# Performance work log

Measured on AMD Instinct MI355X. Metric: run time of the kernel, lower is better.

Reference implementation:

```python
import jax, jax.numpy as jnp
import numpy as np

HIDDEN = 2048
FFN = 1024
NUM_EXPERTS = 64
TOP_K = 8
TOTAL_EXPERTS = NUM_EXPERTS + TOP_K  # trash-can experts appended


def setup_inputs() -> dict:
    key = jax.random.key(0)
    ks = jax.random.split(key, 5)
    hidden_states = jax.random.normal(ks[0], (4, 2048, HIDDEN), dtype=jnp.float32)
    # gate: [total_experts, hidden]
    gate_w = jax.random.normal(ks[1], (TOTAL_EXPERTS, HIDDEN), dtype=jnp.float32) * 0.02
    # OlmoeMLP (SwiGLU): gate_proj, up_proj: [E, hidden, ffn]; down_proj: [E, ffn, hidden]
    w_gate = jax.random.normal(ks[2], (NUM_EXPERTS, HIDDEN, FFN), dtype=jnp.float32) * 0.02
    w_up = jax.random.normal(ks[3], (NUM_EXPERTS, HIDDEN, FFN), dtype=jnp.float32) * 0.02
    w_down = jax.random.normal(ks[4], (NUM_EXPERTS, FFN, HIDDEN), dtype=jnp.float32) * 0.02
    return {"hidden_states": hidden_states, "gate_w": gate_w,
            "w_gate": w_gate, "w_up": w_up, "w_down": w_down}


def _moe_forward(hidden_states, gate_w, w_gate, w_up, w_down):
    b, s, h = hidden_states.shape
    x = hidden_states.reshape(-1, h)  # [T, H]
    router_logits = x @ gate_w.T  # [T, total_experts]
    routing_weights = jax.nn.softmax(router_logits.astype(jnp.float32), axis=-1)
    topk_w, topk_idx = jax.lax.top_k(routing_weights, TOP_K)  # [T, K]
    # norm_topk_prob = False -> no renorm
    topk_w = topk_w.astype(hidden_states.dtype)

    # Dense-equivalent combine honoring sparsity via per-expert mask-weighted sum:
    # combine_w[t, e] = sum of topk weights where topk_idx==e, zero for trash experts.
    onehot = jax.nn.one_hot(topk_idx, TOTAL_EXPERTS, dtype=topk_w.dtype)  # [T,K,E_tot]
    combine_w = jnp.einsum('tk,tke->te', topk_w, onehot)[:, :NUM_EXPERTS]  # [T,E]

    # Grouped expert compute (vectorized over experts).
    # For correctness baseline we compute each expert on all tokens and weight;
    # zero weights kill non-routed tokens (same math as gather/scatter).
    def one_expert(wg, wu, wd, w_col):
        inter = jax.nn.silu(x @ wg) * (x @ wu)  # [T, FFN]
        return (inter @ wd) * w_col[:, None]    # [T, H]

    out = jnp.zeros_like(x)
    # scan over experts to cap peak memory at one [T,FFN] intermediate
    def body(acc, args):
        wg, wu, wd, w_col = args
        return acc + one_expert(wg, wu, wd, w_col), None
    out, _ = jax.lax.scan(body, out, (w_gate, w_up, w_down, combine_w.T))
    return out.reshape(b, s, h), router_logits


def reference(hidden_states, gate_w, w_gate, w_up, w_down):
    return _moe_forward(hidden_states, gate_w, w_gate, w_up, w_down)
```

## Files before the change

### kernel.cpp

```cpp
#include <hip/hip_runtime.h>
#include <hip/hip_bf16.h>
#include <stdint.h>

#define T_TOK 8192
#define HID   2048
#define FFN   1024
#define NEXP  64
#define ETOT  72
#define NPAD  80
#define TOPK  8
#define NASSIGN (T_TOK*TOPK)
#define ECHUNK 16

typedef unsigned short u16;
typedef __bf16 bf16;
typedef bf16 bf16x8 __attribute__((ext_vector_type(8)));
typedef float f32x4 __attribute__((ext_vector_type(4)));

typedef const __attribute__((address_space(1))) void* gp_t;
typedef __attribute__((address_space(3))) void* lp_t;

__device__ __forceinline__ void gload16(const void* g, void* lds) {
  __builtin_amdgcn_global_load_lds((gp_t)g, (lp_t)lds, 16, 0, 0);
}

__device__ __forceinline__ f32x4 mfma16(bf16x8 a, bf16x8 b, f32x4 c) {
  return __builtin_amdgcn_mfma_f32_16x16x32_bf16(a, b, c, 0, 0, 0);
}

union U8 { bf16 h[8]; uint4 u; };
union U2 { bf16 h[2]; unsigned int u; };

__global__ void k_prep_x(const float* __restrict__ x, u16* __restrict__ xh,
                         u16* __restrict__ xl, int n8) {
  int i = blockIdx.x * blockDim.x + threadIdx.x;
  int stride = gridDim.x * blockDim.x;
  for (; i < n8; i += stride) {
    const float4* p = (const float4*)(x + (size_t)i * 8);
    float4 a = p[0], b = p[1];
    float f[8] = {a.x,a.y,a.z,a.w,b.x,b.y,b.z,b.w};
    U8 hh, ll;
#pragma unroll
    for (int j = 0; j < 8; j++) {
      bf16 h = (bf16)f[j];
      hh.h[j] = h;
      ll.h[j] = (bf16)(f[j] - (float)h);
    }
    ((uint4*)xh)[i] = hh.u;
    ((uint4*)xl)[i] = ll.u;
  }
}

__global__ void k_prep_gate(const float* __restrict__ gw, u16* __restrict__ gh,
                            u16* __restrict__ gl) {
  int e = blockIdx.x;
  for (int k8 = threadIdx.x; k8 < HID/8; k8 += blockDim.x) {
    U8 hh, ll;
    if (e < ETOT) {
      const float4* p = (const float4*)(gw + (size_t)e*HID + k8*8);
      float4 a = p[0], b = p[1];
      float f[8] = {a.x,a.y,a.z,a.w,b.x,b.y,b.z,b.w};
#pragma unroll
      for (int j = 0; j < 8; j++) {
        bf16 h = (bf16)f[j]; hh.h[j] = h; ll.h[j] = (bf16)(f[j]-(float)h);
      }
    } else {
      hh.u = make_uint4(0,0,0,0); ll.u = make_uint4(0,0,0,0);
    }
    ((uint4*)gh)[(size_t)e*(HID/8) + k8] = hh.u;
    ((uint4*)gl)[(size_t)e*(HID/8) + k8] = ll.u;
  }
}

__global__ void k_convT(const float* __restrict__ src, u16* __restrict__ dst,
                        int R, int C) {
  int e = blockIdx.z;
  src += (size_t)e * R * C;
  dst += (size_t)e * R * C;
  int c0 = blockIdx.x * 64, r0 = blockIdx.y * 128;
  __shared__ u16 t[64 * 132];
  int tid = threadIdx.x;
  int rr = tid >> 4, cc = (tid & 15) * 4;
#pragma unroll
  for (int it = 0; it < 8; it++) {
    int r = it * 16 + rr;
    float4 v = *(const float4*)(src + (size_t)(r0 + r) * C + c0 + cc);
    const float* f = &v.x;
#pragma unroll
    for (int i = 0; i < 4; i++) {
      U2 u; u.h[0] = (bf16)f[i]; u.h[1] = (bf16)0.f;
      t[(cc + i) * 132 + r] = (u16)(u.u & 0xffffu);
    }
  }
  __syncthreads();
  int n = tid >> 2, kb = (tid & 3) * 32;
  u16* drow = dst + (size_t)(c0 + n) * R + r0 + kb;
  const u16* srow = &t[n * 132 + kb];
#pragma unroll
  for (int j = 0; j < 2; j++) {
    uint2 a = *(const uint2*)&srow[j*16 + 0];
    uint2 b = *(const uint2*)&srow[j*16 + 4];
    uint2 c = *(const uint2*)&srow[j*16 + 8];
    uint2 d = *(const uint2*)&srow[j*16 + 12];
    *(uint4*)&drow[j*16]     = make_uint4(a.x, a.y, b.x, b.y);
    *(uint4*)&drow[j*16 + 8] = make_uint4(c.x, c.y, d.x, d.y);
  }
}

__global__ void k_router(const u16* __restrict__ xh, const u16* __restrict__ xl,
                         const u16* __restrict__ gh, const u16* __restrict__ gl,
                         float* __restrict__ logits_out, int* __restrict__ tk_idx,
                         float* __restrict__ tk_w, int* __restrict__ counts) {
  __shared__ u16 la_h[64*32], la_l[64*32], lb_h[NPAD*32], lb_l[NPAD*32];
  __shared__ float llog[64*NPAD];
  int tid = threadIdx.x, lane = tid & 63, wid = tid >> 6;
  int t0 = blockIdx.x * 64;
  int rsub = lane >> 2, csub = lane & 3;
  f32x4 acc[5] = {};
#pragma unroll 1
  for (int k0 = 0; k0 < HID; k0 += 32) {
    int arow = wid*16 + rsub;
    gload16(xh + (size_t)(t0+arow)*HID + k0 + csub*8, &la_h[wid*512]);
    gload16(xl + (size_t)(t0+arow)*HID + k0 + csub*8, &la_l[wid*512]);
    int brow = wid*16 + rsub;
    gload16(gh + (size_t)brow*HID + k0 + csub*8, &lb_h[wid*512]);
    gload16(gl + (size_t)brow*HID + k0 + csub*8, &lb_l[wid*512]);
    if (wid == 0) gload16(gh + (size_t)(64+rsub)*HID + k0 + csub*8, &lb_h[4*512]);
    if (wid == 1) gload16(gl + (size_t)(64+rsub)*HID + k0 + csub*8, &lb_l[4*512]);
    __syncthreads();
    int ar = wid*16 + (lane & 15);
    int ks = lane >> 4;
    bf16x8 ah = *(const bf16x8*)&la_h[ar*32 + ks*8];
    bf16x8 al = *(const bf16x8*)&la_l[ar*32 + ks*8];
#pragma unroll
    for (int nf = 0; nf < 5; nf++) {
      int br = nf*16 + (lane & 15);
      bf16x8 bh = *(const bf16x8*)&lb_h[br*32 + ks*8];
      bf16x8 bl = *(const bf16x8*)&lb_l[br*32 + ks*8];
      acc[nf] = mfma16(ah, bh, acc[nf]);
      acc[nf] = mfma16(ah, bl, acc[nf]);
      acc[nf] = mfma16(al, bh, acc[nf]);
    }
    __syncthreads();
  }
  {
    int q = lane >> 4, c = lane & 15;
#pragma unroll
    for (int nf = 0; nf < 5; nf++)
#pragma unroll
      for (int r = 0; r < 4; r++)
        llog[(wid*16 + q*4 + r)*NPAD + nf*16 + c] = acc[nf][r];
  }
  __syncthreads();
  if (tid < 64) {
    int t = t0 + tid;
    float* lg = &llog[tid*NPAD];
    float m = -1e30f;
    for (int e = 0; e < ETOT; e++) {
      float v = lg[e];
      logits_out[(size_t)t*ETOT + e] = v;
      m = fmaxf(m, v);
    }
    float s = 0.f;
    for (int e = 0; e < ETOT; e++) s += __expf(lg[e] - m);
    uint64_t m0 = 0; unsigned int m1 = 0;
    for (int k = 0; k < TOPK; k++) {
      float best = -1e30f; int bi = 0;
      for (int e = 0; e < ETOT; e++) {
        bool used = (e < 64) ? ((m0 >> e) & 1) : ((m1 >> (e-64)) & 1);
        float v = lg[e];
        if (!used && v > best) { best = v; bi = e; }
      }
      if (bi < 64) m0 |= (1ull << bi); else m1 |= (1u << (bi-64));
      tk_idx[t*TOPK + k] = bi;
      tk_w[t*TOPK + k] = __expf(best - m) / s;
      if (bi < NEXP) atomicAdd(&counts[bi], 1);
    }
  }
}

__global__ void k_scan(const int* __restrict__ counts, int* __restrict__ offsets,
                       int* __restrict__ cursors) {
  if (threadIdx.x == 0) {
    int s = 0;
    for (int e = 0; e < NEXP; e++) { offsets[e] = s; cursors[e] = s; s += counts[e]; }
  }
}

__global__ void k_build(const int* __restrict__ tk_idx, const float* __restrict__ tk_w,
                        int* __restrict__ cursors, int* __restrict__ rows,
                        float* __restrict__ rwgt) {
  int t = blockIdx.x * blockDim.x + threadIdx.x;
  if (t >= T_TOK) return;
#pragma unroll
  for (int k = 0; k < TOPK; k++) {
    int e = tk_idx[t*TOPK + k];
    if (e < NEXP) {
      int p = atomicAdd(&cursors[e], 1);
      rows[p] = t;
      rwgt[p] = tk_w[t*TOPK + k];
    }
  }
}

__launch_bounds__(256, 2)
__global__ void k_expert_gu(const u16* __restrict__ xh, const u16* __restrict__ wgT,
                            const u16* __restrict__ wuT, const int* __restrict__ counts,
                            const int* __restrict__ offsets, const int* __restrict__ rows,
                            u16* __restrict__ inter, int e0) {
  int ez = blockIdx.z, e = e0 + ez, nb = blockIdx.y;
  int cnt = counts[e];
  if (cnt == 0) return;
  int off = offsets[e];
  int n0 = nb * 128;
  int tid = threadIdx.x, lane = tid & 63, wid = tid >> 6;
  int wm = (wid >> 1) * 64, wn = (wid & 1) * 64;
  __shared__ u16 la[128*32], lbg[128*32], lbu[128*32];
  __shared__ u16 lout[128*128];
  int rsub = lane >> 2, csub = lane & 3;
  int swzc = csub ^ ((rsub >> 1) & 3);
  int nr1 = wid*16 + rsub, nr2 = nr1 + 64;
  const u16* gb_g1 = wgT + ((size_t)ez*FFN + n0 + nr1)*HID + swzc*8;
  const u16* gb_g2 = wgT + ((size_t)ez*FFN + n0 + nr2)*HID + swzc*8;
  const u16* gb_u1 = wuT + ((size_t)ez*FFN + n0 + nr1)*HID + swzc*8;
  const u16* gb_u2 = wuT + ((size_t)ez*FFN + n0 + nr2)*HID + swzc*8;

  for (int m0 = blockIdx.x * 128; m0 < cnt; m0 += gridDim.x * 128) {
    int tok1 = (m0 + nr1 < cnt) ? rows[off + m0 + nr1] : 0;
    int tok2 = (m0 + nr2 < cnt) ? rows[off + m0 + nr2] : 0;
    const u16* ga1 = xh + (size_t)tok1*HID + swzc*8;
    const u16* ga2 = xh + (size_t)tok2*HID + swzc*8;
    f32x4 accg[4][4] = {}, accu[4][4] = {};
#pragma unroll 1
    for (int k0 = 0; k0 < HID; k0 += 32) {
      gload16(ga1 + k0, &la[wid*512]);
      gload16(ga2 + k0, &la[(wid+4)*512]);
      gload16(gb_g1 + k0, &lbg[wid*512]);
      gload16(gb_g2 + k0, &lbg[(wid+4)*512]);
      gload16(gb_u1 + k0, &lbu[wid*512]);
      gload16(gb_u2 + k0, &lbu[(wid+4)*512]);
      __syncthreads();
      bf16x8 afr[4], bgf[4], buf_[4];
#pragma unroll
      for (int i = 0; i < 4; i++) {
        int row = wm + i*16 + (lane & 15);
        int ch = (lane >> 4) ^ ((row >> 1) & 3);
        afr[i] = *(const bf16x8*)&la[row*32 + ch*8];
        int n = wn + i*16 + (lane & 15);
        int chb = (lane >> 4) ^ ((n >> 1) & 3);
        bgf[i]  = *(const bf16x8*)&lbg[n*32 + chb*8];
        buf_[i] = *(const bf16x8*)&lbu[n*32 + chb*8];
      }
#pragma unroll
      for (int nf = 0; nf < 4; nf++)
#pragma unroll
        for (int mf = 0; mf < 4; mf++) {
          accg[mf][nf] = mfma16(afr[mf], bgf[nf], accg[mf][nf]);
          accu[mf][nf] = mfma16(afr[mf], buf_[nf], accu[mf][nf]);
        }
      __syncthreads();
    }
#pragma unroll
    for (int mf = 0; mf < 4; mf++)
#pragma unroll
      for (int nf = 0; nf < 4; nf++)
#pragma unroll
        for (int r = 0; r < 4; r++) {
          float g = accg[mf][nf][r], u = accu[mf][nf][r];
          float v = g / (1.f + __expf(-g)) * u;
          int row = wm + mf*16 + (lane >> 4)*4 + r;
          int col = wn + nf*16 + (lane & 15);
          U2 t; t.h[0] = (bf16)v; t.h[1] = (bf16)0.f;
          lout[row*128 + col] = (u16)(t.u & 0xffffu);
        }
    __syncthreads();
    for (int idx = tid; idx < 2048; idx += 256) {
      int row = idx >> 4, c16 = idx & 15;
      if (m0 + row < cnt) {
        uint4 v = *(const uint4*)&lout[row*128 + c16*8];
        *(uint4*)&inter[(size_t)(off + m0 + row)*FFN + n0 + c16*8] = v;
      }
    }
    __syncthreads();
  }
}

__launch_bounds__(256, 2)
__global__ void k_expert_down(const u16* __restrict__ inter, const u16* __restrict__ wdT,
                              const int* __restrict__ counts, const int* __restrict__ offsets,
                              const int* __restrict__ rows, const float* __restrict__ rwgt,
                              float* __restrict__ out, int e0) {
  int ez = blockIdx.z, e = e0 + ez, nb = blockIdx.y;
  int cnt = counts[e];
  if (cnt == 0) return;
  int off = offsets[e];
  int n0 = nb * 128;
  int tid = threadIdx.x, lane = tid & 63, wid = tid >> 6;
  int wm = (wid >> 1) * 64, wn = (wid & 1) * 64;
  __shared__ u16 la[128*32], lb[128*32];
  __shared__ int rows_l[128];
  __shared__ float rw_l[128];
  int rsub = lane >> 2, csub = lane & 3;
  int swzc = csub ^ ((rsub >> 1) & 3);
  int nr1 = wid*16 + rsub, nr2 = nr1 + 64;
  const u16* gb1 = wdT + ((size_t)ez*HID + n0 + nr1)*FFN + swzc*8;
  const u16* gb2 = wdT + ((size_t)ez*HID + n0 + nr2)*FFN + swzc*8;

  for (int m0 = blockIdx.x * 128; m0 < cnt; m0 += gridDim.x * 128) {
    __syncthreads();
    if (tid < 128) {
      int r = m0 + tid;
      rows_l[tid] = (r < cnt) ? rows[off + r] : 0;
      rw_l[tid]   = (r < cnt) ? rwgt[off + r] : 0.f;
    }
    const u16* ga1 = inter + (size_t)(off + m0 + nr1)*FFN + swzc*8;
    const u16* ga2 = inter + (size_t)(off + m0 + nr2)*FFN + swzc*8;
    f32x4 acc[4][4] = {};
#pragma unroll 1
    for (int k0 = 0; k0 < FFN; k0 += 32) {
      gload16(ga1 + k0, &la[wid*512]);
      gload16(ga2 + k0, &la[(wid+4)*512]);
      gload16(gb1 + k0, &lb[wid*512]);
      gload16(gb2 + k0, &lb[(wid+4)*512]);
      __syncthreads();
      bf16x8 afr[4], bfr[4];
#pragma unroll
      for (int i = 0; i < 4; i++) {
        int row = wm + i*16 + (lane & 15);
        int ch = (lane >> 4) ^ ((row >> 1) & 3);
        afr[i] = *(const bf16x8*)&la[row*32 + ch*8];
        int n = wn + i*16 + (lane & 15);
        int chb = (lane >> 4) ^ ((n >> 1) & 3);
        bfr[i] = *(const bf16x8*)&lb[n*32 + chb*8];
      }
#pragma unroll
      for (int nf = 0; nf < 4; nf++)
#pragma unroll
        for (int mf = 0; mf < 4; mf++)
          acc[mf][nf] = mfma16(afr[mf], bfr[nf], acc[mf][nf]);
      __syncthreads();
    }
#pragma unroll
    for (int mf = 0; mf < 4; mf++)
#pragma unroll
      for (int nf = 0; nf < 4; nf++)
#pragma unroll
        for (int r = 0; r < 4; r++) {
          int row = wm + mf*16 + (lane >> 4)*4 + r;
          if (m0 + row < cnt) {
            int tok = rows_l[row];
            float w = rw_l[row];
            int col = n0 + wn + nf*16 + (lane & 15);
            atomicAdd(&out[(size_t)tok*HID + col], w * acc[mf][nf][r]);
          }
        }
  }
}

extern "C" void kernel_launch(void* const* d_in, const int* in_sizes, int n_in,
                              void* d_out, int out_size, void* d_ws, size_t ws_size,
                              hipStream_t stream) {
  const float* x      = (const float*)d_in[0];
  const float* gate_w = (const float*)d_in[1];
  const float* wg     = (const float*)d_in[2];
  const float* wu     = (const float*)d_in[3];
  const float* wd     = (const float*)d_in[4];
  float* out = (float*)d_out;
  float* logits_out = out + (size_t)T_TOK * HID;

  char* w = (char*)d_ws;
  u16* xh = (u16*)w;            w += (size_t)T_TOK*HID*2;
  u16* xl = (u16*)w;            w += (size_t)T_TOK*HID*2;
  u16* gh = (u16*)w;            w += (size_t)NPAD*HID*2;
  u16* gl = (u16*)w;            w += (size_t)NPAD*HID*2;
  int* tk_idx = (int*)w;        w += (size_t)T_TOK*TOPK*4;
  float* tk_w = (float*)w;      w += (size_t)T_TOK*TOPK*4;
  int* counts = (int*)w;        w += 256;
  int* offsets = (int*)w;       w += 256;
  int* cursors = (int*)w;       w += 256;
  int* rows = (int*)w;          w += (size_t)NASSIGN*4;
  float* rwgt = (float*)w;      w += (size_t)NASSIGN*4;
  u16* inter = (u16*)w;         w += ((size_t)NASSIGN + 128)*FFN*2;
  u16* wgT = (u16*)w;           w += (size_t)ECHUNK*FFN*HID*2;
  u16* wuT = (u16*)w;           w += (size_t)ECHUNK*FFN*HID*2;
  u16* wdT = (u16*)w;

  hipMemsetAsync(d_out, 0, (size_t)T_TOK*HID*4, stream);
  hipMemsetAsync(counts, 0, 256, stream);

  k_prep_x<<<2048, 256, 0, stream>>>(x, xh, xl, T_TOK*HID/8);
  k_prep_gate<<<NPAD, 256, 0, stream>>>(gate_w, gh, gl);
  k_router<<<T_TOK/64, 256, 0, stream>>>(xh, xl, gh, gl, logits_out, tk_idx, tk_w, counts);
  k_scan<<<1, 64, 0, stream>>>(counts, offsets, cursors);
  k_build<<<T_TOK/256, 256, 0, stream>>>(tk_idx, tk_w, cursors, rows, rwgt);

  for (int p = 0; p < NEXP/ECHUNK; p++) {
    int e0 = p * ECHUNK;
    k_convT<<<dim3(FFN/64, HID/128, ECHUNK), 256, 0, stream>>>(
        wg + (size_t)e0*HID*FFN, wgT, HID, FFN);
    k_convT<<<dim3(FFN/64, HID/128, ECHUNK), 256, 0, stream>>>(
        wu + (size_t)e0*HID*FFN, wuT, HID, FFN);
    k_convT<<<dim3(HID/64, FFN/128, ECHUNK), 256, 0, stream>>>(
        wd + (size_t)e0*FFN*HID, wdT, FFN, HID);
    k_expert_gu<<<dim3(8, FFN/128, ECHUNK), 256, 0, stream>>>(
        xh, wgT, wuT, counts, offsets, rows, inter, e0);
    k_expert_down<<<dim3(8, HID/128, ECHUNK), 256, 0, stream>>>(
        inter, wdT, counts, offsets, rows, rwgt, out, e0);
  }
}
```

Baseline: 2.188 ms.

## Double-buffer LDS in expert GEMMs, remap grid, and size expert chunks by workspace

Both expert GEMM kernels now double-buffer their LDS tiles, so the global-to-LDS load for the next K step overlaps MFMA work on the current one, with one barrier per step. The epilogue of the gate/up kernel writes its output in two 64-row passes to keep LDS usage within budget. The grid is flattened so that expert and N-tile share blockIdx.x, ordering work differently. The host picks the expert chunk size from the available workspace, up to all 64 experts at once, which cuts the number of launches. The costs are more LDS per block, a higher launch-bounds occupancy target on the down kernel that may force register spills, and a larger transposed-weight workspace.

Measured after the change: 4.119 ms. 1.88x slower.

```diff
diff --git a/kernel.cpp b/kernel.cpp
--- a/kernel.cpp
+++ b/kernel.cpp
@@ -10,7 +10,6 @@
 #define NPAD  80
 #define TOPK  8
 #define NASSIGN (T_TOK*TOPK)
-#define ECHUNK 16
 
 typedef unsigned short u16;
 typedef __bf16 bf16;
@@ -208,15 +207,17 @@
                             const u16* __restrict__ wuT, const int* __restrict__ counts,
                             const int* __restrict__ offsets, const int* __restrict__ rows,
                             u16* __restrict__ inter, int e0) {
-  int ez = blockIdx.z, e = e0 + ez, nb = blockIdx.y;
+  int g = blockIdx.x;
+  int ez = g >> 3, nb = g & 7;
+  int e = e0 + ez;
   int cnt = counts[e];
   if (cnt == 0) return;
   int off = offsets[e];
   int n0 = nb * 128;
   int tid = threadIdx.x, lane = tid & 63, wid = tid >> 6;
   int wm = (wid >> 1) * 64, wn = (wid & 1) * 64;
-  __shared__ u16 la[128*32], lbg[128*32], lbu[128*32];
-  __shared__ u16 lout[128*128];
+  __shared__ u16 la[2][128*32], lbg[2][128*32], lbu[2][128*32];
+  __shared__ u16 lout[64*128];
   int rsub = lane >> 2, csub = lane & 3;
   int swzc = csub ^ ((rsub >> 1) & 3);
   int nr1 = wid*16 + rsub, nr2 = nr1 + 64;
@@ -225,79 +226,103 @@
   const u16* gb_u1 = wuT + ((size_t)ez*FFN + n0 + nr1)*HID + swzc*8;
   const u16* gb_u2 = wuT + ((size_t)ez*FFN + n0 + nr2)*HID + swzc*8;
 
-  for (int m0 = blockIdx.x * 128; m0 < cnt; m0 += gridDim.x * 128) {
+  for (int m0 = blockIdx.y * 128; m0 < cnt; m0 += gridDim.y * 128) {
     int tok1 = (m0 + nr1 < cnt) ? rows[off + m0 + nr1] : 0;
     int tok2 = (m0 + nr2 < cnt) ? rows[off + m0 + nr2] : 0;
     const u16* ga1 = xh + (size_t)tok1*HID + swzc*8;
     const u16* ga2 = xh + (size_t)tok2*HID + swzc*8;
     f32x4 accg[4][4] = {}, accu[4][4] = {};
-#pragma unroll 1
-    for (int k0 = 0; k0 < HID; k0 += 32) {
-      gload16(ga1 + k0, &la[wid*512]);
-      gload16(ga2 + k0, &la[(wid+4)*512]);
-      gload16(gb_g1 + k0, &lbg[wid*512]);
-      gload16(gb_g2 + k0, &lbg[(wid+4)*512]);
-      gload16(gb_u1 + k0, &lbu[wid*512]);
-      gload16(gb_u2 + k0, &lbu[(wid+4)*512]);
+
+#define GU_STAGE(B, K0) do { \
+      gload16(ga1 + (K0), &la[B][wid*512]); \
+      gload16(ga2 + (K0), &la[B][(wid+4)*512]); \
+      gload16(gb_g1 + (K0), &lbg[B][wid*512]); \
+      gload16(gb_g2 + (K0), &lbg[B][(wid+4)*512]); \
+      gload16(gb_u1 + (K0), &lbu[B][wid*512]); \
+      gload16(gb_u2 + (K0), &lbu[B][(wid+4)*512]); \
+    } while (0)
+
+#define GU_COMPUTE(B) do { \
+      bf16x8 afr[4], bgf[4], buf_[4]; \
+      _Pragma("unroll") \
+      for (int i = 0; i < 4; i++) { \
+        int row = wm + i*16 + (lane & 15); \
+        int ch = (lane >> 4) ^ ((row >> 1) & 3); \
+        afr[i] = *(const bf16x8*)&la[B][row*32 + ch*8]; \
+        int n = wn + i*16 + (lane & 15); \
+        int chb = (lane >> 4) ^ ((n >> 1) & 3); \
+        bgf[i]  = *(const bf16x8*)&lbg[B][n*32 + chb*8]; \
+        buf_[i] = *(const bf16x8*)&lbu[B][n*32 + chb*8]; \
+      } \
+      _Pragma("unroll") \
+      for (int nf = 0; nf < 4; nf++) \
+        _Pragma("unroll") \
+        for (int mf = 0; mf < 4; mf++) { \
+          accg[mf][nf] = mfma16(afr[mf], bgf[nf], accg[mf][nf]); \
+          accu[mf][nf] = mfma16(afr[mf], buf_[nf], accu[mf][nf]); \
+        } \
+    } while (0)
+
+    GU_STAGE(0, 0);
+    __syncthreads();
+    int b = 0;
+#pragma unroll 2
+    for (int k0 = 32; k0 < HID; k0 += 32) {
+      GU_STAGE(b ^ 1, k0);
+      GU_COMPUTE(b);
       __syncthreads();
-      bf16x8 afr[4], bgf[4], buf_[4];
-#pragma unroll
-      for (int i = 0; i < 4; i++) {
-        int row = wm + i*16 + (lane & 15);
-        int ch = (lane >> 4) ^ ((row >> 1) & 3);
-        afr[i] = *(const bf16x8*)&la[row*32 + ch*8];
-        int n = wn + i*16 + (lane & 15);
-        int chb = (lane >> 4) ^ ((n >> 1) & 3);
-        bgf[i]  = *(const bf16x8*)&lbg[n*32 + chb*8];
-        buf_[i] = *(const bf16x8*)&lbu[n*32 + chb*8];
+      b ^= 1;
+    }
+    GU_COMPUTE(b);
+
+#pragma unroll
+    for (int pass = 0; pass < 2; pass++) {
+      if ((wid >> 1) == pass) {
+#pragma unroll
+        for (int mf = 0; mf < 4; mf++)
+#pragma unroll
+          for (int nf = 0; nf < 4; nf++)
+#pragma unroll
+            for (int r = 0; r < 4; r++) {
+              float gg = accg[mf][nf][r], uu = accu[mf][nf][r];
+              float v = gg / (1.f + __expf(-gg)) * uu;
+              int row = mf*16 + (lane >> 4)*4 + r;
+              int col = wn + nf*16 + (lane & 15);
+              U2 t; t.h[0] = (bf16)v; t.h[1] = (bf16)0.f;
+              lout[row*128 + col] = (u16)(t.u & 0xffffu);
+            }
       }
-#pragma unroll
-      for (int nf = 0; nf < 4; nf++)
-#pragma unroll
-        for (int mf = 0; mf < 4; mf++) {
-          accg[mf][nf] = mfma16(afr[mf], bgf[nf], accg[mf][nf]);
-          accu[mf][nf] = mfma16(afr[mf], buf_[nf], accu[mf][nf]);
+      __syncthreads();
+      for (int idx = tid; idx < 1024; idx += 256) {
+        int row = idx >> 4, c16 = idx & 15;
+        int grow = m0 + pass*64 + row;
+        if (grow < cnt) {
+          uint4 v = *(const uint4*)&lout[row*128 + c16*8];
+          *(uint4*)&inter[(size_t)(off + grow)*FFN + n0 + c16*8] = v;
         }
+      }
       __syncthreads();
     }
-#pragma unroll
-    for (int mf = 0; mf < 4; mf++)
-#pragma unroll
-      for (int nf = 0; nf < 4; nf++)
-#pragma unroll
-        for (int r = 0; r < 4; r++) {
-          float g = accg[mf][nf][r], u = accu[mf][nf][r];
-          float v = g / (1.f + __expf(-g)) * u;
-          int row = wm + mf*16 + (lane >> 4)*4 + r;
-          int col = wn + nf*16 + (lane & 15);
-          U2 t; t.h[0] = (bf16)v; t.h[1] = (bf16)0.f;
-          lout[row*128 + col] = (u16)(t.u & 0xffffu);
-        }
-    __syncthreads();
-    for (int idx = tid; idx < 2048; idx += 256) {
-      int row = idx >> 4, c16 = idx & 15;
-      if (m0 + row < cnt) {
-        uint4 v = *(const uint4*)&lout[row*128 + c16*8];
-        *(uint4*)&inter[(size_t)(off + m0 + row)*FFN + n0 + c16*8] = v;
-      }
-    }
-    __syncthreads();
-  }
-}
-
-__launch_bounds__(256, 2)
+  }
+#undef GU_STAGE
+#undef GU_COMPUTE
+}
+
+__launch_bounds__(256, 3)
 __global__ void k_expert_down(const u16* __restrict__ inter, const u16* __restrict__ wdT,
                               const int* __restrict__ counts, const int* __restrict__ offsets,
                               const int* __restrict__ rows, const float* __restrict__ rwgt,
                               float* __restrict__ out, int e0) {
-  int ez = blockIdx.z, e = e0 + ez, nb = blockIdx.y;
+  int g = blockIdx.x;
+  int ez = g >> 4, nb = g & 15;
+  int e = e0 + ez;
   int cnt = counts[e];
   if (cnt == 0) return;
   int off = offsets[e];
   int n0 = nb * 128;
   int tid = threadIdx.x, lane = tid & 63, wid = tid >> 6;
   int wm = (wid >> 1) * 64, wn = (wid & 1) * 64;
-  __shared__ u16 la[128*32], lb[128*32];
+  __shared__ u16 la[2][128*32], lb[2][128*32];
   __shared__ int rows_l[128];
   __shared__ float rw_l[128];
   int rsub = lane >> 2, csub = lane & 3;
@@ -306,8 +331,7 @@
   const u16* gb1 = wdT + ((size_t)ez*HID + n0 + nr1)*FFN + swzc*8;
   const u16* gb2 = wdT + ((size_t)ez*HID + n0 + nr2)*FFN + swzc*8;
 
-  for (int m0 = blockIdx.x * 128; m0 < cnt; m0 += gridDim.x * 128) {
-    __syncthreads();
+  for (int m0 = blockIdx.y * 128; m0 < cnt; m0 += gridDim.y * 128) {
     if (tid < 128) {
       int r = m0 + tid;
       rows_l[tid] = (r < cnt) ? rows[off + r] : 0;
@@ -316,30 +340,44 @@
     const u16* ga1 = inter + (size_t)(off + m0 + nr1)*FFN + swzc*8;
     const u16* ga2 = inter + (size_t)(off + m0 + nr2)*FFN + swzc*8;
     f32x4 acc[4][4] = {};
-#pragma unroll 1
-    for (int k0 = 0; k0 < FFN; k0 += 32) {
-      gload16(ga1 + k0, &la[wid*512]);
-      gload16(ga2 + k0, &la[(wid+4)*512]);
-      gload16(gb1 + k0, &lb[wid*512]);
-      gload16(gb2 + k0, &lb[(wid+4)*512]);
+
+#define DN_STAGE(B, K0) do { \
+      gload16(ga1 + (K0), &la[B][wid*512]); \
+      gload16(ga2 + (K0), &la[B][(wid+4)*512]); \
+      gload16(gb1 + (K0), &lb[B][wid*512]); \
+      gload16(gb2 + (K0), &lb[B][(wid+4)*512]); \
+    } while (0)
+
+#define DN_COMPUTE(B) do { \
+      bf16x8 afr[4], bfr[4]; \
+      _Pragma("unroll") \
+      for (int i = 0; i < 4; i++) { \
+        int row = wm + i*16 + (lane & 15); \
+        int ch = (lane >> 4) ^ ((row >> 1) & 3); \
+        afr[i] = *(const bf16x8*)&la[B][row*32 + ch*8]; \
+        int n = wn + i*16 + (lane & 15); \
+        int chb = (lane >> 4) ^ ((n >> 1) & 3); \
+        bfr[i] = *(const bf16x8*)&lb[B][n*32 + chb*8]; \
+      } \
+      _Pragma("unroll") \
+      for (int nf = 0; nf < 4; nf++) \
+        _Pragma("unroll") \
+        for (int mf = 0; mf < 4; mf++) \
+          acc[mf][nf] = mfma16(afr[mf], bfr[nf], acc[mf][nf]); \
+    } while (0)
+
+    DN_STAGE(0, 0);
+    __syncthreads();
+    int b = 0;
+#pragma unroll 2
+    for (int k0 = 32; k0 < FFN; k0 += 32) {
+      DN_STAGE(b ^ 1, k0);
+      DN_COMPUTE(b);
       __syncthreads();
-      bf16x8 afr[4], bfr[4];
-#pragma unroll
-      for (int i = 0; i < 4; i++) {
-        int row = wm + i*16 + (lane & 15);
-        int ch = (lane >> 4) ^ ((row >> 1) & 3);
-        afr[i] = *(const bf16x8*)&la[row*32 + ch*8];
-        int n = wn + i*16 + (lane & 15);
-        int chb = (lane >> 4) ^ ((n >> 1) & 3);
-        bfr[i] = *(const bf16x8*)&lb[n*32 + chb*8];
-      }
-#pragma unroll
-      for (int nf = 0; nf < 4; nf++)
-#pragma unroll
-        for (int mf = 0; mf < 4; mf++)
-          acc[mf][nf] = mfma16(afr[mf], bfr[nf], acc[mf][nf]);
-      __syncthreads();
-    }
+      b ^= 1;
+    }
+    DN_COMPUTE(b);
+
 #pragma unroll
     for (int mf = 0; mf < 4; mf++)
 #pragma unroll
@@ -354,7 +392,10 @@
             atomicAdd(&out[(size_t)tok*HID + col], w * acc[mf][nf][r]);
           }
         }
-  }
+    __syncthreads();
+  }
+#undef DN_STAGE
+#undef DN_COMPUTE
 }
 
 extern "C" void kernel_launch(void* const* d_in, const int* in_sizes, int n_in,
@@ -381,8 +422,16 @@
   int* rows = (int*)w;          w += (size_t)NASSIGN*4;
   float* rwgt = (float*)w;      w += (size_t)NASSIGN*4;
   u16* inter = (u16*)w;         w += ((size_t)NASSIGN + 128)*FFN*2;
-  u16* wgT = (u16*)w;           w += (size_t)ECHUNK*FFN*HID*2;
-  u16* wuT = (u16*)w;           w += (size_t)ECHUNK*FFN*HID*2;
+  size_t base_used = (size_t)(w - (char*)d_ws);
+
+  size_t per_chunk_full = (size_t)NEXP*FFN*HID*2;
+  int ech;
+  if (ws_size >= base_used + 3*per_chunk_full) ech = NEXP;
+  else if (ws_size >= base_used + 3*(per_chunk_full/2)) ech = NEXP/2;
+  else ech = NEXP/4;
+
+  u16* wgT = (u16*)w;           w += (size_t)ech*FFN*HID*2;
+  u16* wuT = (u16*)w;           w += (size_t)ech*FFN*HID*2;
   u16* wdT = (u16*)w;
 
   hipMemsetAsync(d_out, 0, (size_t)T_TOK*HID*4, stream);
@@ -394,17 +443,16 @@
   k_scan<<<1, 64, 0, stream>>>(counts, offsets, cursors);
   k_build<<<T_TOK/256, 256, 0, stream>>>(tk_idx, tk_w, cursors, rows, rwgt);
 
-  for (int p = 0; p < NEXP/ECHUNK; p++) {
-    int e0 = p * ECHUNK;
-    k_convT<<<dim3(FFN/64, HID/128, ECHUNK), 256, 0, stream>>>(
+  for (int e0 = 0; e0 < NEXP; e0 += ech) {
+    k_convT<<<dim3(FFN/64, HID/128, ech), 256, 0, stream>>>(
         wg + (size_t)e0*HID*FFN, wgT, HID, FFN);
-    k_convT<<<dim3(FFN/64, HID/128, ECHUNK), 256, 0, stream>>>(
+    k_convT<<<dim3(FFN/64, HID/128, ech), 256, 0, stream>>>(
         wu + (size_t)e0*HID*FFN, wuT, HID, FFN);
-    k_convT<<<dim3(HID/64, FFN/128, ECHUNK), 256, 0, stream>>>(
+    k_convT<<<dim3(HID/64, FFN/128, ech), 256, 0, stream>>>(
         wd + (size_t)e0*FFN*HID, wdT, FFN, HID);
-    k_expert_gu<<<dim3(8, FFN/128, ECHUNK), 256, 0, stream>>>(
+    k_expert_gu<<<dim3(ech*(FFN/128), 8, 1), 256, 0, stream>>>(
         xh, wgT, wuT, counts, offsets, rows, inter, e0);
-    k_expert_down<<<dim3(8, HID/128, ECHUNK), 256, 0, stream>>>(
+    k_expert_down<<<dim3(ech*(HID/128), 8, 1), 256, 0, stream>>>(
         inter, wdT, counts, offsets, rows, rwgt, out, e0);
   }
 }
```

## Launch all experts in one grid with XCD-aware block mapping

Applied to the files above, without the earlier changes.

Replaces the four-chunk loop of transpose plus expert launches with one full-size transpose of every expert's weights and single 4096-block launches of the gate/up and down kernels. Block ids are remapped so that all tiles of one expert land on the same XCD, which should improve L2 reuse of that expert's weights. The gate/up kernel halves its output staging buffer by writing in two passes, and both kernels raise their launch-bounds occupancy targets. The cost is a workspace large enough for all 64 experts' transposed weights, and tighter register limits that could cause spills.

Result: faster. 2.051 ms (-6.3%).

```diff
diff --git a/kernel.cpp b/kernel.cpp
--- a/kernel.cpp
+++ b/kernel.cpp
@@ -10,7 +10,6 @@
 #define NPAD  80
 #define TOPK  8
 #define NASSIGN (T_TOK*TOPK)
-#define ECHUNK 16
 
 typedef unsigned short u16;
 typedef __bf16 bf16;
@@ -23,7 +22,6 @@
 __device__ __forceinline__ void gload16(const void* g, void* lds) {
   __builtin_amdgcn_global_load_lds((gp_t)g, (lp_t)lds, 16, 0, 0);
 }
-
 __device__ __forceinline__ f32x4 mfma16(bf16x8 a, bf16x8 b, f32x4 c) {
   return __builtin_amdgcn_mfma_f32_16x16x32_bf16(a, b, c, 0, 0, 0);
 }
@@ -203,12 +201,16 @@
   }
 }
 
-__launch_bounds__(256, 2)
+__launch_bounds__(256, 3)
 __global__ void k_expert_gu(const u16* __restrict__ xh, const u16* __restrict__ wgT,
                             const u16* __restrict__ wuT, const int* __restrict__ counts,
                             const int* __restrict__ offsets, const int* __restrict__ rows,
-                            u16* __restrict__ inter, int e0) {
-  int ez = blockIdx.z, e = e0 + ez, nb = blockIdx.y;
+                            u16* __restrict__ inter) {
+  int wgid = blockIdx.x;
+  int xcd = wgid & 7, slot = wgid >> 3;
+  int m = slot & 7, q = slot >> 3;
+  int g = xcd * 64 + q;
+  int e = g >> 3, nb = g & 7;
   int cnt = counts[e];
   if (cnt == 0) return;
   int off = offsets[e];
@@ -216,16 +218,16 @@
   int tid = threadIdx.x, lane = tid & 63, wid = tid >> 6;
   int wm = (wid >> 1) * 64, wn = (wid & 1) * 64;
   __shared__ u16 la[128*32], lbg[128*32], lbu[128*32];
-  __shared__ u16 lout[128*128];
+  __shared__ u16 lout[64*128];
   int rsub = lane >> 2, csub = lane & 3;
   int swzc = csub ^ ((rsub >> 1) & 3);
   int nr1 = wid*16 + rsub, nr2 = nr1 + 64;
-  const u16* gb_g1 = wgT + ((size_t)ez*FFN + n0 + nr1)*HID + swzc*8;
-  const u16* gb_g2 = wgT + ((size_t)ez*FFN + n0 + nr2)*HID + swzc*8;
-  const u16* gb_u1 = wuT + ((size_t)ez*FFN + n0 + nr1)*HID + swzc*8;
-  const u16* gb_u2 = wuT + ((size_t)ez*FFN + n0 + nr2)*HID + swzc*8;
-
-  for (int m0 = blockIdx.x * 128; m0 < cnt; m0 += gridDim.x * 128) {
+  const u16* gb_g1 = wgT + ((size_t)e*FFN + n0 + nr1)*HID + swzc*8;
+  const u16* gb_g2 = wgT + ((size_t)e*FFN + n0 + nr2)*HID + swzc*8;
+  const u16* gb_u1 = wuT + ((size_t)e*FFN + n0 + nr1)*HID + swzc*8;
+  const u16* gb_u2 = wuT + ((size_t)e*FFN + n0 + nr2)*HID + swzc*8;
+
+  for (int m0 = m * 128; m0 < cnt; m0 += 1024) {
     int tok1 = (m0 + nr1 < cnt) ? rows[off + m0 + nr1] : 0;
     int tok2 = (m0 + nr2 < cnt) ? rows[off + m0 + nr2] : 0;
     const u16* ga1 = xh + (size_t)tok1*HID + swzc*8;
@@ -261,36 +263,46 @@
       __syncthreads();
     }
 #pragma unroll
-    for (int mf = 0; mf < 4; mf++)
-#pragma unroll
-      for (int nf = 0; nf < 4; nf++)
-#pragma unroll
-        for (int r = 0; r < 4; r++) {
-          float g = accg[mf][nf][r], u = accu[mf][nf][r];
-          float v = g / (1.f + __expf(-g)) * u;
-          int row = wm + mf*16 + (lane >> 4)*4 + r;
-          int col = wn + nf*16 + (lane & 15);
-          U2 t; t.h[0] = (bf16)v; t.h[1] = (bf16)0.f;
-          lout[row*128 + col] = (u16)(t.u & 0xffffu);
+    for (int pass = 0; pass < 2; pass++) {
+      if ((wid >> 1) == pass) {
+#pragma unroll
+        for (int mf = 0; mf < 4; mf++)
+#pragma unroll
+          for (int nf = 0; nf < 4; nf++)
+#pragma unroll
+            for (int r = 0; r < 4; r++) {
+              float gg = accg[mf][nf][r], uu = accu[mf][nf][r];
+              float v = gg / (1.f + __expf(-gg)) * uu;
+              int row = mf*16 + (lane >> 4)*4 + r;
+              int col = wn + nf*16 + (lane & 15);
+              U2 t; t.h[0] = (bf16)v; t.h[1] = (bf16)0.f;
+              lout[row*128 + col] = (u16)(t.u & 0xffffu);
+            }
+      }
+      __syncthreads();
+      for (int idx = tid; idx < 1024; idx += 256) {
+        int row = idx >> 4, c16 = idx & 15;
+        int grow = m0 + pass*64 + row;
+        if (grow < cnt) {
+          uint4 v = *(const uint4*)&lout[row*128 + c16*8];
+          *(uint4*)&inter[(size_t)(off + grow)*FFN + n0 + c16*8] = v;
         }
-    __syncthreads();
-    for (int idx = tid; idx < 2048; idx += 256) {
-      int row = idx >> 4, c16 = idx & 15;
-      if (m0 + row < cnt) {
-        uint4 v = *(const uint4*)&lout[row*128 + c16*8];
-        *(uint4*)&inter[(size_t)(off + m0 + row)*FFN + n0 + c16*8] = v;
-      }
-    }
-    __syncthreads();
-  }
-}
-
-__launch_bounds__(256, 2)
+      }
+      __syncthreads();
+    }
+  }
+}
+
+__launch_bounds__(256, 4)
 __global__ void k_expert_down(const u16* __restrict__ inter, const u16* __restrict__ wdT,
                               const int* __restrict__ counts, const int* __restrict__ offsets,
                               const int* __restrict__ rows, const float* __restrict__ rwgt,
-                              float* __restrict__ out, int e0) {
-  int ez = blockIdx.z, e = e0 + ez, nb = blockIdx.y;
+                              float* __restrict__ out) {
+  int wgid = blockIdx.x;
+  int xcd = wgid & 7, slot = wgid >> 3;
+  int m = slot & 3, q = slot >> 2;
+  int g = xcd * 128 + q;
+  int e = g >> 4, nb = g & 15;
   int cnt = counts[e];
   if (cnt == 0) return;
   int off = offsets[e];
@@ -303,10 +315,10 @@
   int rsub = lane >> 2, csub = lane & 3;
   int swzc = csub ^ ((rsub >> 1) & 3);
   int nr1 = wid*16 + rsub, nr2 = nr1 + 64;
-  const u16* gb1 = wdT + ((size_t)ez*HID + n0 + nr1)*FFN + swzc*8;
-  const u16* gb2 = wdT + ((size_t)ez*HID + n0 + nr2)*FFN + swzc*8;
-
-  for (int m0 = blockIdx.x * 128; m0 < cnt; m0 += gridDim.x * 128) {
+  const u16* gb1 = wdT + ((size_t)e*HID + n0 + nr1)*FFN + swzc*8;
+  const u16* gb2 = wdT + ((size_t)e*HID + n0 + nr2)*FFN + swzc*8;
+
+  for (int m0 = m * 128; m0 < cnt; m0 += 512) {
     __syncthreads();
     if (tid < 128) {
       int r = m0 + tid;
@@ -380,9 +392,9 @@
   int* cursors = (int*)w;       w += 256;
   int* rows = (int*)w;          w += (size_t)NASSIGN*4;
   float* rwgt = (float*)w;      w += (size_t)NASSIGN*4;
-  u16* inter = (u16*)w;         w += ((size_t)NASSIGN + 128)*FFN*2;
-  u16* wgT = (u16*)w;           w += (size_t)ECHUNK*FFN*HID*2;
-  u16* wuT = (u16*)w;           w += (size_t)ECHUNK*FFN*HID*2;
+  u16* inter = (u16*)w;         w += ((size_t)NASSIGN + 256)*FFN*2;
+  u16* wgT = (u16*)w;           w += (size_t)NEXP*FFN*HID*2;
+  u16* wuT = (u16*)w;           w += (size_t)NEXP*FFN*HID*2;
   u16* wdT = (u16*)w;
 
   hipMemsetAsync(d_out, 0, (size_t)T_TOK*HID*4, stream);
@@ -394,17 +406,10 @@
   k_scan<<<1, 64, 0, stream>>>(counts, offsets, cursors);
   k_build<<<T_TOK/256, 256, 0, stream>>>(tk_idx, tk_w, cursors, rows, rwgt);
 
-  for (int p = 0; p < NEXP/ECHUNK; p++) {
-    int e0 = p * ECHUNK;
-    k_convT<<<dim3(FFN/64, HID/128, ECHUNK), 256, 0, stream>>>(
-        wg + (size_t)e0*HID*FFN, wgT, HID, FFN);
-    k_convT<<<dim3(FFN/64, HID/128, ECHUNK), 256, 0, stream>>>(
-        wu + (size_t)e0*HID*FFN, wuT, HID, FFN);
-    k_convT<<<dim3(HID/64, FFN/128, ECHUNK), 256, 0, stream>>>(
-        wd + (size_t)e0*FFN*HID, wdT, FFN, HID);
-    k_expert_gu<<<dim3(8, FFN/128, ECHUNK), 256, 0, stream>>>(
-        xh, wgT, wuT, counts, offsets, rows, inter, e0);
-    k_expert_down<<<dim3(8, HID/128, ECHUNK), 256, 0, stream>>>(
-        inter, wdT, counts, offsets, rows, rwgt, out, e0);
-  }
-}
+  k_convT<<<dim3(FFN/64, HID/128, NEXP), 256, 0, stream>>>(wg, wgT, HID, FFN);
+  k_convT<<<dim3(FFN/64, HID/128, NEXP), 256, 0, stream>>>(wu, wuT, HID, FFN);
+  k_convT<<<dim3(HID/64, FFN/128, NEXP), 256, 0, stream>>>(wd, wdT, FFN, HID);
+
+  k_expert_gu<<<4096, 256, 0, stream>>>(xh, wgT, wuT, counts, offsets, rows, inter);
+  k_expert_down<<<4096, 256, 0, stream>>>(inter, wdT, counts, offsets, rows, rwgt, out);
+}
```
